# Kernel optimization log

Hardware: AMD Instinct MI355X
Metric: run time of the kernel (lower is better)

Reference implementation:

```python
import jax, jax.numpy as jnp
import numpy as np

D_MODEL = 1024
NUM_HEADS = 16
D_K = D_MODEL // NUM_HEADS
B, SQ, SK = 2, 2048, 2048


def setup_inputs() -> dict:
    key = jax.random.key(0)
    ks = jax.random.split(key, 12)
    s = 1.0 / np.sqrt(D_MODEL)
    inp = {
        'query': jax.random.normal(ks[0], (B, SQ, D_MODEL), jnp.float32),
        'key': jax.random.normal(ks[1], (B, SK, D_MODEL), jnp.float32),
        'value': jax.random.normal(ks[2], (B, SK, D_MODEL), jnp.float32),
        # causal mask [B, 1, Sq, Sk], True = keep
        'mask': jnp.broadcast_to(jnp.tril(jnp.ones((SQ, SK), bool))[None, None], (B, 1, SQ, SK)),
        'Wq': jax.random.uniform(ks[3], (D_MODEL, D_MODEL), jnp.float32, -s, s),
        'bq': jnp.zeros((D_MODEL,), jnp.float32),
        'Wk': jax.random.uniform(ks[4], (D_MODEL, D_MODEL), jnp.float32, -s, s),
        'bk': jnp.zeros((D_MODEL,), jnp.float32),
        'Wv': jax.random.uniform(ks[5], (D_MODEL, D_MODEL), jnp.float32, -s, s),
        'bv': jnp.zeros((D_MODEL,), jnp.float32),
        'Wo': jax.random.uniform(ks[6], (D_MODEL, D_MODEL), jnp.float32, -s, s),
        'bo': jnp.zeros((D_MODEL,), jnp.float32),
    }
    return inp


def reference(query, key, value, mask, Wq, bq, Wk, bk, Wv, bv, Wo, bo):
    b, sq, _ = query.shape
    sk = key.shape[1]
    # projections; torch Linear: x @ W.T + b (here W stored as [in, out] so x @ W)
    Q = (query @ Wq + bq).reshape(b, sq, NUM_HEADS, D_K).transpose(0, 2, 1, 3)  # [B,H,Sq,dk]
    K = (key @ Wk + bk).reshape(b, sk, NUM_HEADS, D_K).transpose(0, 2, 1, 3)
    V = (value @ Wv + bv).reshape(b, sk, NUM_HEADS, D_K).transpose(0, 2, 1, 3)
    scores = jnp.einsum('bhqd,bhkd->bhqk', Q, K) / jnp.sqrt(jnp.float32(D_K))
    neg = jnp.finfo(scores.dtype).min
    scores = jnp.where(mask, scores, neg)
    probs = jax.nn.softmax(scores, axis=-1)
    attn = jnp.einsum('bhqk,bhkd->bhqd', probs, V)  # [B,H,Sq,dk]
    attn = attn.transpose(0, 2, 1, 3).reshape(b, sq, D_MODEL)
    return attn @ Wo + bo
```

## Files before the change

### kernel.cpp

```cpp
#include <hip/hip_runtime.h>
#include <hip/hip_bf16.h>

#define DM 1024
#define NH 16
#define DKK 64
#define NB 2
#define SQL 2048
#define SKL 2048

typedef __attribute__((ext_vector_type(8))) short short8;
typedef __attribute__((ext_vector_type(4))) float floatx4;

static __device__ inline floatx4 mfma16(short8 a, short8 b, floatx4 c) {
    return __builtin_amdgcn_mfma_f32_16x16x32_bf16(a, b, c, 0, 0, 0);
}

static __device__ inline unsigned short f2bf(float f) {
    __hip_bfloat16 h = __float2bfloat16(f);
    return *reinterpret_cast<unsigned short*>(&h);
}

__device__ __forceinline__ void gload16(const void* g, void* l) {
    __builtin_amdgcn_global_load_lds(
        (const __attribute__((address_space(1))) void*)g,
        (__attribute__((address_space(3))) void*)l, 16, 0, 0);
}

__global__ __launch_bounds__(256) void x2bf(
    const float* __restrict__ q, const float* __restrict__ k, const float* __restrict__ v,
    unsigned short* __restrict__ oq, unsigned short* __restrict__ ok, unsigned short* __restrict__ ov)
{
    const int n4 = 1 << 20;
    for (int i = blockIdx.x * blockDim.x + threadIdx.x; i < 3 * n4; i += gridDim.x * blockDim.x) {
        const int z = i >> 20, off = (i & (n4 - 1)) * 4;
        const float* src = z == 0 ? q : (z == 1 ? k : v);
        unsigned short* dst = z == 0 ? oq : (z == 1 ? ok : ov);
        const float4 f = *reinterpret_cast<const float4*>(&src[off]);
        uint2 p;
        p.x = (unsigned)f2bf(f.x) | ((unsigned)f2bf(f.y) << 16);
        p.y = (unsigned)f2bf(f.z) | ((unsigned)f2bf(f.w) << 16);
        *reinterpret_cast<uint2*>(&dst[off]) = p;
    }
}

__global__ void transpose_w4(const float* __restrict__ Wq, const float* __restrict__ Wk,
                             const float* __restrict__ Wv, const float* __restrict__ Wo,
                             unsigned short* __restrict__ WtQ, unsigned short* __restrict__ WtK,
                             unsigned short* __restrict__ WtV, unsigned short* __restrict__ WtO) {
    const int z = blockIdx.z;
    const float* W = z == 0 ? Wq : (z == 1 ? Wk : (z == 2 ? Wv : Wo));
    unsigned short* Wt = z == 0 ? WtQ : (z == 1 ? WtK : (z == 2 ? WtV : WtO));
    __shared__ unsigned short t[32][33];
    int tx = threadIdx.x, ty = threadIdx.y;
    int n0 = blockIdx.x * 32, k0 = blockIdx.y * 32;
#pragma unroll
    for (int i = 0; i < 4; i++) {
        int k = k0 + ty + i * 8;
        t[tx][ty + i * 8] = f2bf(W[k * DM + n0 + tx]);
    }
    __syncthreads();
#pragma unroll
    for (int i = 0; i < 4; i++) {
        int n = n0 + ty + i * 8;
        Wt[n * DM + k0 + tx] = t[ty + i * 8][tx];
    }
}

__global__ __launch_bounds__(256) void proj_qkv2(
    const unsigned short* __restrict__ Xq, const unsigned short* __restrict__ Xk,
    const unsigned short* __restrict__ Xv,
    const unsigned short* __restrict__ WtQ, const unsigned short* __restrict__ WtK,
    const unsigned short* __restrict__ WtV,
    const float* __restrict__ bq, const float* __restrict__ bk, const float* __restrict__ bv,
    unsigned short* __restrict__ Qh, unsigned short* __restrict__ Kh, unsigned short* __restrict__ Vt)
{
    const int z = blockIdx.z;
    const unsigned short* X  = z == 0 ? Xq : (z == 1 ? Xk : Xv);
    const unsigned short* Wt = z == 0 ? WtQ : (z == 1 ? WtK : WtV);
    const float* bias = z == 0 ? bq : (z == 1 ? bk : bv);
    unsigned short* out = z == 0 ? Qh : (z == 1 ? Kh : Vt);

    __shared__ __align__(16) unsigned short As[128 * 64];
    __shared__ __align__(16) unsigned short Bs[128 * 64];

    const int tid = threadIdx.x;
    const int w = tid >> 6, lane = tid & 63;
    const int lg = lane >> 4, lr = lane & 15;
    const int wr = w >> 1, wc = w & 1;
    const int m0 = blockIdx.x * 128, n0 = blockIdx.y * 128;

    floatx4 acc[4][4] = {};

    int srow[4], scol[4], ldsoff[4];
#pragma unroll
    for (int i = 0; i < 4; i++) {
        const int idx = i * 256 + tid;
        srow[i] = idx >> 3;
        scol[i] = ((idx & 7) ^ (srow[i] & 7)) * 8;
        ldsoff[i] = (i * 256 + w * 64) * 8;
    }

    for (int k0 = 0; k0 < DM; k0 += 64) {
        __syncthreads();
#pragma unroll
        for (int i = 0; i < 4; i++)
            gload16(&X[(size_t)(m0 + srow[i]) * DM + k0 + scol[i]], &As[ldsoff[i]]);
#pragma unroll
        for (int i = 0; i < 4; i++)
            gload16(&Wt[(size_t)(n0 + srow[i]) * DM + k0 + scol[i]], &Bs[ldsoff[i]]);
        __syncthreads();
#pragma unroll
        for (int kk = 0; kk < 2; kk++) {
            short8 a[4], b[4];
#pragma unroll
            for (int mi = 0; mi < 4; mi++) {
                const int r = wr * 64 + mi * 16 + lr;
                a[mi] = *reinterpret_cast<const short8*>(&As[r * 64 + (((kk * 4 + lg) ^ (r & 7)) * 8)]);
            }
#pragma unroll
            for (int ni = 0; ni < 4; ni++) {
                const int r = wc * 64 + ni * 16 + lr;
                b[ni] = *reinterpret_cast<const short8*>(&Bs[r * 64 + (((kk * 4 + lg) ^ (r & 7)) * 8)]);
            }
#pragma unroll
            for (int mi = 0; mi < 4; mi++)
#pragma unroll
                for (int ni = 0; ni < 4; ni++)
                    acc[mi][ni] = mfma16(a[mi], b[ni], acc[mi][ni]);
        }
    }

    const float qscale = (z == 0) ? 0.125f : 1.0f;
#pragma unroll
    for (int mi = 0; mi < 4; mi++)
#pragma unroll
        for (int ni = 0; ni < 4; ni++)
#pragma unroll
            for (int r = 0; r < 4; r++) {
                const int m = m0 + wr * 64 + mi * 16 + lg * 4 + r;
                const int n = n0 + wc * 64 + ni * 16 + lr;
                const float val = (acc[mi][ni][r] + bias[n]) * qscale;
                const int bb = m >> 11, s = m & 2047;
                const int h = n >> 6, d = n & 63;
                const unsigned short o = f2bf(val);
                if (z != 2)
                    out[(((size_t)(bb * NH + h) * SQL) + s) * DKK + d] = o;
                else
                    out[(((size_t)(bb * NH + h) * DKK) + d) * SKL + s] = o;
            }
}

#define KVB 64

__device__ __forceinline__ void load_tile(uint4* kr, uint4* vr,
    const unsigned short* __restrict__ Kb, const unsigned short* __restrict__ Vb,
    int kv0, int tid)
{
    const int row = tid >> 3, sl = tid & 7;
    *kr = *reinterpret_cast<const uint4*>(&Kb[(size_t)(kv0 + row) * DKK + sl * 8]);
    *vr = *reinterpret_cast<const uint4*>(&Vb[(size_t)row * SKL + kv0 + sl * 8]);
}

__device__ __forceinline__ void store_tile(unsigned short* kl, unsigned short* vl,
                                           const uint4* kr, const uint4* vr, int tid)
{
    const int row = tid >> 3, sl = tid & 7;
    const int off = row * 64 + ((sl ^ (row & 7)) * 8);
    *reinterpret_cast<uint4*>(&kl[off]) = *kr;
    *reinterpret_cast<uint4*>(&vl[off]) = *vr;
}

__global__ __launch_bounds__(512) void attn_fwd(
    const unsigned short* __restrict__ Qh, const unsigned short* __restrict__ Kh,
    const unsigned short* __restrict__ Vt, unsigned short* __restrict__ attn)
{
    __shared__ __align__(16) unsigned short Kl[2][4096];
    __shared__ __align__(16) unsigned short Vl[2][4096];
    __shared__ __align__(16) unsigned short Pl[8][1024];

    const int tid = threadIdx.x;
    const int w = tid >> 6, lane = tid & 63;
    const int lg = lane >> 4, lr = lane & 15;
    const int b = blockIdx.z, h = blockIdx.y;
    const int q0 = (int)(gridDim.x - 1 - blockIdx.x) * 128;
    const int wq0 = q0 + w * 16;

    const unsigned short* Qb = Qh + (size_t)(b * NH + h) * SQL * DKK;
    const unsigned short* Kb = Kh + (size_t)(b * NH + h) * SKL * DKK;
    const unsigned short* Vb = Vt + (size_t)(b * NH + h) * DKK * SKL;

    short8 qf[2];
#pragma unroll
    for (int kk = 0; kk < 2; kk++)
        qf[kk] = *reinterpret_cast<const short8*>(
            &Qb[(size_t)(wq0 + lr) * DKK + kk * 32 + lg * 8]);

    floatx4 oa[4] = {};
    float m_s = -1e30f, l_s = 0.f;

    const int nt = (q0 >> 6) + 2;

    uint4 kr, vr;
    load_tile(&kr, &vr, Kb, Vb, 0, tid);

    for (int t = 0; t < nt; ++t) {
        const int kv0 = t << 6;
        const int cur = t & 1;
        store_tile(Kl[cur], Vl[cur], &kr, &vr, tid);
        __syncthreads();
        if (t + 1 < nt) load_tile(&kr, &vr, Kb, Vb, kv0 + KVB, tid);

        if (kv0 < wq0 + 16) {
            floatx4 sa[4] = {};
            __builtin_amdgcn_s_setprio(1);
#pragma unroll
            for (int c = 0; c < 4; c++) {
                const int row = c * 16 + lr;
#pragma unroll
                for (int kk = 0; kk < 2; kk++) {
                    short8 kf = *reinterpret_cast<const short8*>(
                        &Kl[cur][row * 64 + (((kk * 4 + lg) ^ (lr & 7)) * 8)]);
                    sa[c] = mfma16(kf, qf[kk], sa[c]);
                }
            }
            __builtin_amdgcn_s_setprio(0);

            const bool do_mask = (kv0 + KVB - 1 > wq0);
            const int q = wq0 + lr;
            float pm = -1e30f;
#pragma unroll
            for (int c = 0; c < 4; c++)
#pragma unroll
                for (int r = 0; r < 4; r++) {
                    float v = sa[c][r];
                    if (do_mask && (kv0 + c * 16 + lg * 4 + r > q)) v = -1e30f;
                    sa[c][r] = v;
                    pm = fmaxf(pm, v);
                }
            pm = fmaxf(pm, __shfl_xor(pm, 16));
            pm = fmaxf(pm, __shfl_xor(pm, 32));
            if (!__all(pm <= m_s + 8.f)) {
                const float mn = fmaxf(m_s, pm);
                const float es = __expf(m_s - mn);
                m_s = mn;
                l_s *= es;
#pragma unroll
                for (int f = 0; f < 4; f++)
#pragma unroll
                    for (int r = 0; r < 4; r++)
                        oa[f][r] *= es;
            }
            float ps = 0.f;
#pragma unroll
            for (int c = 0; c < 4; c++)
#pragma unroll
                for (int r = 0; r < 4; r++) {
                    float p = __expf(sa[c][r] - m_s);
                    sa[c][r] = p;
                    ps += p;
                }
            ps += __shfl_xor(ps, 16);
            ps += __shfl_xor(ps, 32);
            l_s += ps;
#pragma unroll
            for (int c = 0; c < 4; c++) {
                uint2 pk;
                pk.x = (unsigned)f2bf(sa[c][0]) | ((unsigned)f2bf(sa[c][1]) << 16);
                pk.y = (unsigned)f2bf(sa[c][2]) | ((unsigned)f2bf(sa[c][3]) << 16);
                *reinterpret_cast<uint2*>(
                    &Pl[w][lr * 64 + (((c * 2 + (lg >> 1)) ^ (lr & 7)) * 8) + (lg & 1) * 4]) = pk;
            }
            short8 pf[2];
#pragma unroll
            for (int kk = 0; kk < 2; kk++)
                pf[kk] = *reinterpret_cast<const short8*>(
                    &Pl[w][lr * 64 + (((kk * 4 + lg) ^ (lr & 7)) * 8)]);
            __builtin_amdgcn_s_setprio(1);
#pragma unroll
            for (int f = 0; f < 4; f++) {
                const int row = f * 16 + lr;
#pragma unroll
                for (int kk = 0; kk < 2; kk++) {
                    short8 vt = *reinterpret_cast<const short8*>(
                        &Vl[cur][row * 64 + (((kk * 4 + lg) ^ (lr & 7)) * 8)]);
                    oa[f] = mfma16(vt, pf[kk], oa[f]);
                }
            }
            __builtin_amdgcn_s_setprio(0);
        }
    }

    {
        const float inv = 1.f / l_s;
#pragma unroll
        for (int f = 0; f < 4; f++) {
            uint2 pk;
            pk.x = (unsigned)f2bf(oa[f][0] * inv) | ((unsigned)f2bf(oa[f][1] * inv) << 16);
            pk.y = (unsigned)f2bf(oa[f][2] * inv) | ((unsigned)f2bf(oa[f][3] * inv) << 16);
            *reinterpret_cast<uint2*>(
                &Pl[w][lr * 64 + (((f * 2 + (lg >> 1)) ^ (lr & 7)) * 8) + (lg & 1) * 4]) = pk;
        }
    }
#pragma unroll
    for (int i = 0; i < 2; i++) {
        const int rl = i * 8 + (lane >> 3);
        const int slot = lane & 7;
        const uint4 o = *reinterpret_cast<const uint4*>(
            &Pl[w][rl * 64 + ((slot ^ (rl & 7)) * 8)]);
        const int q = wq0 + rl;
        *reinterpret_cast<uint4*>(
            &attn[((size_t)(b * SQL + q)) * DM + h * DKK + slot * 8]) = o;
    }
}

__global__ __launch_bounds__(256) void proj_o2(
    const unsigned short* __restrict__ Attn, const unsigned short* __restrict__ WtO,
    const float* __restrict__ bo, float* __restrict__ out)
{
    __shared__ __align__(16) unsigned short As[128 * 64];
    __shared__ __align__(16) unsigned short Bs[64 * 64];

    const int tid = threadIdx.x;
    const int w = tid >> 6, lane = tid & 63;
    const int lg = lane >> 4, lr = lane & 15;
    const int wr = w >> 1, wc = w & 1;
    const int m0 = blockIdx.x * 128, n0 = blockIdx.y * 64;

    floatx4 acc[4][2] = {};

    int srow[4], scol[4], ldsoff[4];
#pragma unroll
    for (int i = 0; i < 4; i++) {
        const int idx = i * 256 + tid;
        srow[i] = idx >> 3;
        scol[i] = ((idx & 7) ^ (srow[i] & 7)) * 8;
        ldsoff[i] = (i * 256 + w * 64) * 8;
    }

    for (int k0 = 0; k0 < DM; k0 += 64) {
        __syncthreads();
#pragma unroll
        for (int i = 0; i < 4; i++)
            gload16(&Attn[(size_t)(m0 + srow[i]) * DM + k0 + scol[i]], &As[ldsoff[i]]);
#pragma unroll
        for (int i = 0; i < 2; i++)
            gload16(&WtO[(size_t)(n0 + srow[i]) * DM + k0 + scol[i]], &Bs[ldsoff[i]]);
        __syncthreads();
#pragma unroll
        for (int kk = 0; kk < 2; kk++) {
            short8 a[4], b[2];
#pragma unroll
            for (int mi = 0; mi < 4; mi++) {
                const int r = wr * 64 + mi * 16 + lr;
                a[mi] = *reinterpret_cast<const short8*>(&As[r * 64 + (((kk * 4 + lg) ^ (r & 7)) * 8)]);
            }
#pragma unroll
            for (int ni = 0; ni < 2; ni++) {
                const int r = wc * 32 + ni * 16 + lr;
                b[ni] = *reinterpret_cast<const short8*>(&Bs[r * 64 + (((kk * 4 + lg) ^ (r & 7)) * 8)]);
            }
#pragma unroll
            for (int mi = 0; mi < 4; mi++)
#pragma unroll
                for (int ni = 0; ni < 2; ni++)
                    acc[mi][ni] = mfma16(a[mi], b[ni], acc[mi][ni]);
        }
    }

#pragma unroll
    for (int mi = 0; mi < 4; mi++)
#pragma unroll
        for (int ni = 0; ni < 2; ni++)
#pragma unroll
            for (int r = 0; r < 4; r++) {
                const int m = m0 + wr * 64 + mi * 16 + lg * 4 + r;
                const int n = n0 + wc * 32 + ni * 16 + lr;
                out[(size_t)m * DM + n] = acc[mi][ni][r] + bo[n];
            }
}

extern "C" void kernel_launch(void* const* d_in, const int* in_sizes, int n_in,
                              void* d_out, int out_size, void* d_ws, size_t ws_size,
                              hipStream_t stream) {
    const float* query = (const float*)d_in[0];
    const float* key   = (const float*)d_in[1];
    const float* value = (const float*)d_in[2];
    const float* Wq = (const float*)d_in[4];
    const float* bq = (const float*)d_in[5];
    const float* Wk = (const float*)d_in[6];
    const float* bk = (const float*)d_in[7];
    const float* Wv = (const float*)d_in[8];
    const float* bv = (const float*)d_in[9];
    const float* Wo = (const float*)d_in[10];
    const float* bo = (const float*)d_in[11];
    float* out = (float*)d_out;

    unsigned short* ws = (unsigned short*)d_ws;
    const size_t MW = (size_t)DM * DM;
    const size_t MH = (size_t)NB * NH * SQL * DKK;
    unsigned short* WtQ = ws;
    unsigned short* WtK = WtQ + MW;
    unsigned short* WtV = WtK + MW;
    unsigned short* WtO = WtV + MW;
    unsigned short* Qh  = WtO + MW;
    unsigned short* Kh  = Qh + MH;
    unsigned short* Vt  = Kh + MH;
    unsigned short* At  = Vt + MH;
    unsigned short* Xbq = (unsigned short*)d_out;
    unsigned short* Xbk = Xbq + MH;
    unsigned short* Xbv = At;

    x2bf<<<2048, 256, 0, stream>>>(query, key, value, Xbq, Xbk, Xbv);
    transpose_w4<<<dim3(32, 32, 4), dim3(32, 8), 0, stream>>>(Wq, Wk, Wv, Wo, WtQ, WtK, WtV, WtO);
    proj_qkv2<<<dim3(32, 8, 3), 256, 0, stream>>>(Xbq, Xbk, Xbv, WtQ, WtK, WtV,
                                                  bq, bk, bv, Qh, Kh, Vt);
    attn_fwd<<<dim3(SQL / 128, NH, NB), 512, 0, stream>>>(Qh, Kh, Vt, At);
    proj_o2<<<dim3(32, 16), 256, 0, stream>>>(At, WtO, bo, out);
}
```

Measured before the change: 264.2 us.

## Use 128-wide KV tiles, exp2 softmax with folded log2e scale, lazy row reductions

The attention kernel now stages 128 keys per iteration (two 64-key subtiles) in larger double-buffered LDS tiles, which halves the number of barriers and tile loads. The Q scale folds in log2(e) so the softmax can use exp2 directly. The row max is only shuffle-reduced when a rescale is needed, and the row sum is kept per lane and reduced once at the end. In exchange it doubles K/V LDS use, which may cut occupancy, and causal tiles waste more work on the diagonal.

```diff
diff --git a/kernel.cpp b/kernel.cpp
--- a/kernel.cpp
+++ b/kernel.cpp
@@ -1,5 +1,6 @@
 #include <hip/hip_runtime.h>
 #include <hip/hip_bf16.h>
+#include <math.h>
 
 #define DM 1024
 #define NH 16
@@ -19,6 +20,8 @@
     __hip_bfloat16 h = __float2bfloat16(f);
     return *reinterpret_cast<unsigned short*>(&h);
 }
+
+static __device__ inline float fexp2(float x) { return exp2f(x); }
 
 __device__ __forceinline__ void gload16(const void* g, void* l) {
     __builtin_amdgcn_global_load_lds(
@@ -130,7 +133,7 @@
         }
     }
 
-    const float qscale = (z == 0) ? 0.125f : 1.0f;
+    const float qscale = (z == 0) ? 0.18033688f : 1.0f;
 #pragma unroll
     for (int mi = 0; mi < 4; mi++)
 #pragma unroll
@@ -150,32 +153,42 @@
             }
 }
 
-#define KVB 64
+#define KVB 128
 
 __device__ __forceinline__ void load_tile(uint4* kr, uint4* vr,
     const unsigned short* __restrict__ Kb, const unsigned short* __restrict__ Vb,
     int kv0, int tid)
 {
-    const int row = tid >> 3, sl = tid & 7;
-    *kr = *reinterpret_cast<const uint4*>(&Kb[(size_t)(kv0 + row) * DKK + sl * 8]);
-    *vr = *reinterpret_cast<const uint4*>(&Vb[(size_t)row * SKL + kv0 + sl * 8]);
+#pragma unroll
+    for (int it = 0; it < 2; ++it) {
+        const int ik = it * 512 + tid;
+        const int krow = ik >> 3, ksl = ik & 7;
+        kr[it] = *reinterpret_cast<const uint4*>(&Kb[(size_t)(kv0 + krow) * DKK + ksl * 8]);
+        const int vrow = ik >> 4, vsl = ik & 15;
+        vr[it] = *reinterpret_cast<const uint4*>(&Vb[(size_t)vrow * SKL + kv0 + vsl * 8]);
+    }
 }
 
 __device__ __forceinline__ void store_tile(unsigned short* kl, unsigned short* vl,
                                            const uint4* kr, const uint4* vr, int tid)
 {
-    const int row = tid >> 3, sl = tid & 7;
-    const int off = row * 64 + ((sl ^ (row & 7)) * 8);
-    *reinterpret_cast<uint4*>(&kl[off]) = *kr;
-    *reinterpret_cast<uint4*>(&vl[off]) = *vr;
+#pragma unroll
+    for (int it = 0; it < 2; ++it) {
+        const int ik = it * 512 + tid;
+        const int krow = ik >> 3, ksl = ik & 7;
+        *reinterpret_cast<uint4*>(&kl[krow * 64 + ((ksl ^ (krow & 7)) * 8)]) = kr[it];
+        const int vrow = ik >> 4, vsl = ik & 15;
+        *reinterpret_cast<uint4*>(
+            &vl[vrow * 128 + (((vsl & 8) + ((vsl & 7) ^ (vrow & 7))) * 8)]) = vr[it];
+    }
 }
 
 __global__ __launch_bounds__(512) void attn_fwd(
     const unsigned short* __restrict__ Qh, const unsigned short* __restrict__ Kh,
     const unsigned short* __restrict__ Vt, unsigned short* __restrict__ attn)
 {
-    __shared__ __align__(16) unsigned short Kl[2][4096];
-    __shared__ __align__(16) unsigned short Vl[2][4096];
+    __shared__ __align__(16) unsigned short Kl[2][8192];
+    __shared__ __align__(16) unsigned short Vl[2][8192];
     __shared__ __align__(16) unsigned short Pl[8][1024];
 
     const int tid = threadIdx.x;
@@ -196,110 +209,115 @@
             &Qb[(size_t)(wq0 + lr) * DKK + kk * 32 + lg * 8]);
 
     floatx4 oa[4] = {};
-    float m_s = -1e30f, l_s = 0.f;
-
-    const int nt = (q0 >> 6) + 2;
-
-    uint4 kr, vr;
-    load_tile(&kr, &vr, Kb, Vb, 0, tid);
+    float m_s = -1e30f, l_lane = 0.f;
+
+    const int nt = (q0 >> 7) + 1;
+
+    uint4 kr[2], vr[2];
+    load_tile(kr, vr, Kb, Vb, 0, tid);
 
     for (int t = 0; t < nt; ++t) {
-        const int kv0 = t << 6;
+        const int kv0 = t << 7;
         const int cur = t & 1;
-        store_tile(Kl[cur], Vl[cur], &kr, &vr, tid);
+        store_tile(Kl[cur], Vl[cur], kr, vr, tid);
         __syncthreads();
-        if (t + 1 < nt) load_tile(&kr, &vr, Kb, Vb, kv0 + KVB, tid);
-
-        if (kv0 < wq0 + 16) {
-            floatx4 sa[4] = {};
-            __builtin_amdgcn_s_setprio(1);
-#pragma unroll
-            for (int c = 0; c < 4; c++) {
-                const int row = c * 16 + lr;
-#pragma unroll
-                for (int kk = 0; kk < 2; kk++) {
-                    short8 kf = *reinterpret_cast<const short8*>(
-                        &Kl[cur][row * 64 + (((kk * 4 + lg) ^ (lr & 7)) * 8)]);
-                    sa[c] = mfma16(kf, qf[kk], sa[c]);
-                }
-            }
-            __builtin_amdgcn_s_setprio(0);
-
-            const bool do_mask = (kv0 + KVB - 1 > wq0);
-            const int q = wq0 + lr;
-            float pm = -1e30f;
-#pragma unroll
-            for (int c = 0; c < 4; c++)
-#pragma unroll
-                for (int r = 0; r < 4; r++) {
-                    float v = sa[c][r];
-                    if (do_mask && (kv0 + c * 16 + lg * 4 + r > q)) v = -1e30f;
-                    sa[c][r] = v;
-                    pm = fmaxf(pm, v);
-                }
-            pm = fmaxf(pm, __shfl_xor(pm, 16));
-            pm = fmaxf(pm, __shfl_xor(pm, 32));
-            if (!__all(pm <= m_s + 8.f)) {
-                const float mn = fmaxf(m_s, pm);
-                const float es = __expf(m_s - mn);
-                m_s = mn;
-                l_s *= es;
-#pragma unroll
-                for (int f = 0; f < 4; f++)
-#pragma unroll
-                    for (int r = 0; r < 4; r++)
-                        oa[f][r] *= es;
-            }
-            float ps = 0.f;
-#pragma unroll
-            for (int c = 0; c < 4; c++)
-#pragma unroll
-                for (int r = 0; r < 4; r++) {
-                    float p = __expf(sa[c][r] - m_s);
-                    sa[c][r] = p;
-                    ps += p;
-                }
-            ps += __shfl_xor(ps, 16);
-            ps += __shfl_xor(ps, 32);
-            l_s += ps;
-#pragma unroll
-            for (int c = 0; c < 4; c++) {
-                uint2 pk;
-                pk.x = (unsigned)f2bf(sa[c][0]) | ((unsigned)f2bf(sa[c][1]) << 16);
-                pk.y = (unsigned)f2bf(sa[c][2]) | ((unsigned)f2bf(sa[c][3]) << 16);
-                *reinterpret_cast<uint2*>(
-                    &Pl[w][lr * 64 + (((c * 2 + (lg >> 1)) ^ (lr & 7)) * 8) + (lg & 1) * 4]) = pk;
-            }
-            short8 pf[2];
-#pragma unroll
-            for (int kk = 0; kk < 2; kk++)
-                pf[kk] = *reinterpret_cast<const short8*>(
-                    &Pl[w][lr * 64 + (((kk * 4 + lg) ^ (lr & 7)) * 8)]);
-            __builtin_amdgcn_s_setprio(1);
-#pragma unroll
-            for (int f = 0; f < 4; f++) {
-                const int row = f * 16 + lr;
-#pragma unroll
-                for (int kk = 0; kk < 2; kk++) {
-                    short8 vt = *reinterpret_cast<const short8*>(
-                        &Vl[cur][row * 64 + (((kk * 4 + lg) ^ (lr & 7)) * 8)]);
-                    oa[f] = mfma16(vt, pf[kk], oa[f]);
-                }
-            }
-            __builtin_amdgcn_s_setprio(0);
+        if (t + 1 < nt) load_tile(kr, vr, Kb, Vb, kv0 + KVB, tid);
+
+#pragma unroll
+        for (int sub = 0; sub < 2; ++sub) {
+            const int kvs = kv0 + sub * 64;
+            if (kvs < wq0 + 16) {
+                floatx4 sa[4] = {};
+                __builtin_amdgcn_s_setprio(1);
+#pragma unroll
+                for (int c = 0; c < 4; c++) {
+                    const int row = sub * 64 + c * 16 + lr;
+#pragma unroll
+                    for (int kk = 0; kk < 2; kk++) {
+                        short8 kf = *reinterpret_cast<const short8*>(
+                            &Kl[cur][row * 64 + (((kk * 4 + lg) ^ (lr & 7)) * 8)]);
+                        sa[c] = mfma16(kf, qf[kk], sa[c]);
+                    }
+                }
+                __builtin_amdgcn_s_setprio(0);
+
+                const int q = wq0 + lr;
+                if (kvs + 63 > wq0) {
+#pragma unroll
+                    for (int c = 0; c < 4; c++)
+#pragma unroll
+                        for (int r = 0; r < 4; r++)
+                            if (kvs + c * 16 + lg * 4 + r > q) sa[c][r] = -1e30f;
+                }
+                float cm[4];
+#pragma unroll
+                for (int c = 0; c < 4; c++)
+                    cm[c] = fmaxf(fmaxf(sa[c][0], sa[c][1]), fmaxf(sa[c][2], sa[c][3]));
+                const float pm = fmaxf(fmaxf(cm[0], cm[1]), fmaxf(cm[2], cm[3]));
+                if (!__all(pm <= m_s + 11.5f)) {
+                    float pg = fmaxf(pm, __shfl_xor(pm, 16));
+                    pg = fmaxf(pg, __shfl_xor(pg, 32));
+                    const float mn = fmaxf(m_s, pg);
+                    const float es = fexp2(m_s - mn);
+                    m_s = mn;
+                    l_lane *= es;
+#pragma unroll
+                    for (int f = 0; f < 4; f++)
+#pragma unroll
+                        for (int r = 0; r < 4; r++)
+                            oa[f][r] *= es;
+                }
+                float sc[4];
+#pragma unroll
+                for (int c = 0; c < 4; c++) {
+                    const float p0 = fexp2(sa[c][0] - m_s);
+                    const float p1 = fexp2(sa[c][1] - m_s);
+                    const float p2 = fexp2(sa[c][2] - m_s);
+                    const float p3 = fexp2(sa[c][3] - m_s);
+                    sa[c][0] = p0; sa[c][1] = p1; sa[c][2] = p2; sa[c][3] = p3;
+                    sc[c] = (p0 + p1) + (p2 + p3);
+                }
+                l_lane += (sc[0] + sc[1]) + (sc[2] + sc[3]);
+#pragma unroll
+                for (int c = 0; c < 4; c++) {
+                    uint2 pk;
+                    pk.x = (unsigned)f2bf(sa[c][0]) | ((unsigned)f2bf(sa[c][1]) << 16);
+                    pk.y = (unsigned)f2bf(sa[c][2]) | ((unsigned)f2bf(sa[c][3]) << 16);
+                    *reinterpret_cast<uint2*>(
+                        &Pl[w][lr * 64 + (((c * 2 + (lg >> 1)) ^ (lr & 7)) * 8) + (lg & 1) * 4]) = pk;
+                }
+                short8 pf[2];
+#pragma unroll
+                for (int kk = 0; kk < 2; kk++)
+                    pf[kk] = *reinterpret_cast<const short8*>(
+                        &Pl[w][lr * 64 + (((kk * 4 + lg) ^ (lr & 7)) * 8)]);
+                __builtin_amdgcn_s_setprio(1);
+#pragma unroll
+                for (int f = 0; f < 4; f++) {
+                    const int row = f * 16 + lr;
+#pragma unroll
+                    for (int kk = 0; kk < 2; kk++) {
+                        short8 vt = *reinterpret_cast<const short8*>(
+                            &Vl[cur][row * 128 + (((sub * 8 + kk * 4 + lg) ^ (row & 7)) * 8)]);
+                        oa[f] = mfma16(vt, pf[kk], oa[f]);
+                    }
+                }
+                __builtin_amdgcn_s_setprio(0);
+            }
         }
     }
 
-    {
-        const float inv = 1.f / l_s;
-#pragma unroll
-        for (int f = 0; f < 4; f++) {
-            uint2 pk;
-            pk.x = (unsigned)f2bf(oa[f][0] * inv) | ((unsigned)f2bf(oa[f][1] * inv) << 16);
-            pk.y = (unsigned)f2bf(oa[f][2] * inv) | ((unsigned)f2bf(oa[f][3] * inv) << 16);
-            *reinterpret_cast<uint2*>(
-                &Pl[w][lr * 64 + (((f * 2 + (lg >> 1)) ^ (lr & 7)) * 8) + (lg & 1) * 4]) = pk;
-        }
+    float lt = l_lane + __shfl_xor(l_lane, 16);
+    lt += __shfl_xor(lt, 32);
+    const float inv = 1.f / lt;
+
+#pragma unroll
+    for (int f = 0; f < 4; f++) {
+        uint2 pk;
+        pk.x = (unsigned)f2bf(oa[f][0] * inv) | ((unsigned)f2bf(oa[f][1] * inv) << 16);
+        pk.y = (unsigned)f2bf(oa[f][2] * inv) | ((unsigned)f2bf(oa[f][3] * inv) << 16);
+        *reinterpret_cast<uint2*>(
+            &Pl[w][lr * 64 + (((f * 2 + (lg >> 1)) ^ (lr & 7)) * 8) + (lg & 1) * 4]) = pk;
     }
 #pragma unroll
     for (int i = 0; i < 2; i++) {
```

Result: slower. 300.4 us (+13.7%).
